# Optimization experiments

Hardware: AMD Instinct MI355X
Metric: run time of the kernel (lower is better)

The kernel has to match this reference:

```python
import jax, jax.numpy as jnp
import numpy as np

N_NODES = 50000
N_EDGES = 1600000
IN_FEATS = 128
HID = 128
HEADS = 4
F_HEAD = HID // HEADS  # 32
NEG_SLOPE = 0.2


def setup_inputs() -> dict:
    key = jax.random.key(0)
    ks = jax.random.split(key, 7)
    feat = jax.random.normal(ks[0], (N_NODES, IN_FEATS), dtype=jnp.float32)
    # Xavier-ish scaling for the shared fc weight
    W = jax.random.normal(ks[1], (IN_FEATS, HID), dtype=jnp.float32) * (1.0 / np.sqrt(IN_FEATS))
    attn_l = jax.random.normal(ks[2], (HEADS, F_HEAD), dtype=jnp.float32) * 0.1
    attn_r = jax.random.normal(ks[3], (HEADS, F_HEAD), dtype=jnp.float32) * 0.1
    bias = jnp.zeros((HID,), dtype=jnp.float32)
    src_idx = jax.random.randint(ks[4], (N_EDGES,), 0, N_NODES, dtype=jnp.int32)
    dst_idx = jax.random.randint(ks[5], (N_EDGES,), 0, N_NODES, dtype=jnp.int32)
    return {"feat": feat, "W": W, "attn_l": attn_l, "attn_r": attn_r,
            "bias": bias, "src_idx": src_idx, "dst_idx": dst_idx}


def reference(feat, W, attn_l, attn_r, bias, src_idx, dst_idx):
    N = feat.shape[0]
    # shared linear projection, split into heads: [N, H, F]
    ft = (feat @ W).reshape(N, HEADS, F_HEAD)
    # per-node attention logits: [N, H]
    el = jnp.einsum('nhf,hf->nh', ft, attn_l)
    er = jnp.einsum('nhf,hf->nh', ft, attn_r)
    # per-edge unnormalized score: [E, H]
    e = jax.nn.leaky_relu(el[src_idx] + er[dst_idx], negative_slope=NEG_SLOPE)
    # numerically stable edge softmax grouped by destination node
    m = jax.ops.segment_max(e, dst_idx, num_segments=N)          # [N, H]
    m = jnp.where(jnp.isfinite(m), m, 0.0)                       # guard empty dst
    a = jnp.exp(e - m[dst_idx])                                  # [E, H]
    s = jax.ops.segment_sum(a, dst_idx, num_segments=N)          # [N, H]
    alpha = a / jnp.where(s[dst_idx] > 0, s[dst_idx], 1.0)       # [E, H]
    # weighted scatter-sum aggregation: [N, H, F]
    msgs = ft[src_idx] * alpha[:, :, None]
    out = jax.ops.segment_sum(msgs, dst_idx, num_segments=N)
    out = out + bias.reshape(1, HEADS, F_HEAD)
    return out.reshape(N, HEADS * F_HEAD)  # flatten(1)
```

## Files before the change

### kernel.cpp

```cpp
#include <hip/hip_runtime.h>
#include <hip/hip_bf16.h>
#include <math.h>

#define NEG_SLOPE 0.2f
#define NBMAX 1024
#define CAP 4096
#define CH 8192

typedef __attribute__((ext_vector_type(8))) short short8;
typedef __attribute__((ext_vector_type(4))) float f32x4;
union BU { uint4 u; short8 s; };

__device__ __forceinline__ unsigned bf16rne(float f) {
    unsigned u = __float_as_uint(f);
    return (u + 0x7fffu + ((u >> 16) & 1u)) >> 16;
}
__device__ __forceinline__ short bf16s(float f) { return (short)bf16rne(f); }

__global__ __launch_bounds__(256) void k_wprep(
    const float* __restrict__ W, const float* __restrict__ attn_l,
    const float* __restrict__ attn_r, uint4* __restrict__ Wfrag,
    float4* __restrict__ WL, float4* __restrict__ WR,
    int* __restrict__ gcur, int NB) {
    int tid = blockIdx.x * 256 + threadIdx.x;
    if (tid < 2048) {
        int lane = tid & 63;
        int ki = (tid >> 6) & 3;
        int t = (tid >> 8) & 3;
        int cg = tid >> 10;
        int col = cg * 64 + t * 16 + (lane & 15);
        int kb = ki * 32 + (lane >> 4) * 8;
        unsigned d[4];
#pragma unroll
        for (int p = 0; p < 4; ++p) {
            unsigned lo = bf16rne(W[(kb + 2 * p) * 128 + col]);
            unsigned hi = bf16rne(W[(kb + 2 * p + 1) * 128 + col]);
            d[p] = lo | (hi << 16);
        }
        Wfrag[tid] = make_uint4(d[0], d[1], d[2], d[3]);
    } else if (tid < 2048 + 128) {
        int k = tid - 2048;
        const float* wr_ = W + k * 128;
        float l0 = 0, l1 = 0, l2 = 0, l3 = 0, r0 = 0, r1 = 0, r2 = 0, r3 = 0;
        for (int j = 0; j < 32; ++j) {
            l0 += wr_[j] * attn_l[j];
            l1 += wr_[32 + j] * attn_l[32 + j];
            l2 += wr_[64 + j] * attn_l[64 + j];
            l3 += wr_[96 + j] * attn_l[96 + j];
            r0 += wr_[j] * attn_r[j];
            r1 += wr_[32 + j] * attn_r[32 + j];
            r2 += wr_[64 + j] * attn_r[64 + j];
            r3 += wr_[96 + j] * attn_r[96 + j];
        }
        WL[k] = make_float4(l0, l1, l2, l3);
        WR[k] = make_float4(r0, r1, r2, r3);
    } else if (tid - 2176 < NB) {
        gcur[tid - 2176] = 0;
    }
}

__global__ __launch_bounds__(256) void k_fc(
    const float* __restrict__ feat, const uint4* __restrict__ Wfrag,
    const f32x4* __restrict__ WL, const f32x4* __restrict__ WR,
    unsigned* __restrict__ ftbf, float* __restrict__ el, float* __restrict__ er,
    int N) {
    __shared__ f32x4 WLs[128], WRs[128];
    int tid = threadIdx.x;
    if (tid < 128) WLs[tid] = WL[tid];
    else WRs[tid - 128] = WR[tid - 128];
    __syncthreads();
    const int wave = tid >> 6, lane = tid & 63;
    const int rt = wave & 1, cg = wave >> 1;
    const int nbase = blockIdx.x * 32 + rt * 16;
    const int row = nbase + (lane & 15);
    const int rowc = min(row, N - 1);
    const int q = lane >> 4;

    BU b[4][4];
#pragma unroll
    for (int t = 0; t < 4; ++t)
#pragma unroll
        for (int ki = 0; ki < 4; ++ki)
            b[t][ki].u = Wfrag[cg * 1024 + t * 256 + ki * 64 + lane];

    f32x4 acc0 = {0, 0, 0, 0}, acc1 = {0, 0, 0, 0}, acc2 = {0, 0, 0, 0}, acc3 = {0, 0, 0, 0};
    f32x4 elacc = {0, 0, 0, 0}, eracc = {0, 0, 0, 0};
    const float* fr = feat + (size_t)rowc * 128;
#pragma unroll
    for (int ki = 0; ki < 4; ++ki) {
        float4 f0 = *(const float4*)(fr + ki * 32 + q * 8);
        float4 f1 = *(const float4*)(fr + ki * 32 + q * 8 + 4);
        short8 a;
        a[0] = bf16s(f0.x); a[1] = bf16s(f0.y); a[2] = bf16s(f0.z); a[3] = bf16s(f0.w);
        a[4] = bf16s(f1.x); a[5] = bf16s(f1.y); a[6] = bf16s(f1.z); a[7] = bf16s(f1.w);
        acc0 = __builtin_amdgcn_mfma_f32_16x16x32_bf16(a, b[0][ki].s, acc0, 0, 0, 0);
        acc1 = __builtin_amdgcn_mfma_f32_16x16x32_bf16(a, b[1][ki].s, acc1, 0, 0, 0);
        acc2 = __builtin_amdgcn_mfma_f32_16x16x32_bf16(a, b[2][ki].s, acc2, 0, 0, 0);
        acc3 = __builtin_amdgcn_mfma_f32_16x16x32_bf16(a, b[3][ki].s, acc3, 0, 0, 0);
        if (cg == 0) {
            int kb = ki * 32 + q * 8;
            elacc += f0.x * WLs[kb + 0]; eracc += f0.x * WRs[kb + 0];
            elacc += f0.y * WLs[kb + 1]; eracc += f0.y * WRs[kb + 1];
            elacc += f0.z * WLs[kb + 2]; eracc += f0.z * WRs[kb + 2];
            elacc += f0.w * WLs[kb + 3]; eracc += f0.w * WRs[kb + 3];
            elacc += f1.x * WLs[kb + 4]; eracc += f1.x * WRs[kb + 4];
            elacc += f1.y * WLs[kb + 5]; eracc += f1.y * WRs[kb + 5];
            elacc += f1.z * WLs[kb + 6]; eracc += f1.z * WRs[kb + 6];
            elacc += f1.w * WLs[kb + 7]; eracc += f1.w * WRs[kb + 7];
        }
    }
#pragma unroll
    for (int t = 0; t < 4; ++t) {
#pragma unroll
        for (int r = 0; r < 4; ++r) {
            float d = (t == 0) ? acc0[r] : (t == 1) ? acc1[r] : (t == 2) ? acc2[r] : acc3[r];
            unsigned m = bf16rne(d);
            unsigned nb = (unsigned)__shfl_xor((int)m, 1, 64);
            int node = nbase + q * 4 + r;
            if (!(lane & 1) && node < N)
                ftbf[(size_t)node * 64 + cg * 32 + t * 8 + ((lane & 15) >> 1)] = m | (nb << 16);
        }
    }
    if (cg == 0) {
#pragma unroll
        for (int c = 0; c < 4; ++c) {
            elacc[c] += __shfl_xor(elacc[c], 16, 64);
            eracc[c] += __shfl_xor(eracc[c], 16, 64);
            elacc[c] += __shfl_xor(elacc[c], 32, 64);
            eracc[c] += __shfl_xor(eracc[c], 32, 64);
        }
        if (lane < 16 && row < N) {
            *(float4*)(el + (size_t)row * 4) = make_float4(elacc[0], elacc[1], elacc[2], elacc[3]);
            *(float4*)(er + (size_t)row * 4) = make_float4(eracc[0], eracc[1], eracc[2], eracc[3]);
        }
    }
}

__global__ __launch_bounds__(1024) void k_scatter_b(
    const int* __restrict__ src, const int* __restrict__ dst,
    int* __restrict__ gcur, unsigned* __restrict__ B, int E, int NB) {
    __shared__ int h[NBMAX];
    __shared__ int lc[NBMAX];
    int tid = threadIdx.x;
    for (int t = tid; t < NB; t += 1024) h[t] = 0;
    __syncthreads();
    int beg = blockIdx.x * CH;
    int end = min(beg + CH, E);
    for (int i = beg + tid; i < end; i += 1024) atomicAdd(&h[dst[i] >> 6], 1);
    __syncthreads();
    for (int t = tid; t < NB; t += 1024)
        lc[t] = (h[t] > 0) ? atomicAdd(&gcur[t], h[t]) : 0;
    __syncthreads();
    for (int i = beg + tid; i < end; i += 1024) {
        int d = dst[i];
        int pos = atomicAdd(&lc[d >> 6], 1);
        if (pos < CAP)
            B[(size_t)(d >> 6) * CAP + pos] = ((unsigned)src[i] << 6) | (unsigned)(d & 63);
    }
}

__global__ __launch_bounds__(256) void k_sort(
    const unsigned* __restrict__ B, const int* __restrict__ gcur,
    int* __restrict__ srt, uint2* __restrict__ od, int N) {
    __shared__ int hist[64];
    __shared__ int cur[64];
    const int tid = threadIdx.x;
    const int b = blockIdx.x;
    const int m = min(gcur[b], CAP);
    const size_t base = (size_t)b * CAP;
    if (tid < 64) hist[tid] = 0;
    __syncthreads();
    for (int i = tid; i < m; i += 256) atomicAdd(&hist[B[base + i] & 63], 1);
    __syncthreads();
    int v0 = (tid < 64) ? hist[tid] : 0;
    for (int off = 1; off < 64; off <<= 1) {
        int t = (tid < 64 && tid >= off) ? hist[tid - off] : 0;
        __syncthreads();
        if (tid < 64) hist[tid] += t;
        __syncthreads();
    }
    if (tid < 64) {
        int ex = hist[tid] - v0;
        cur[tid] = ex;
        int node = (b << 6) + tid;
        if (node < N) od[node] = make_uint2((unsigned)(base + ex), (unsigned)v0);
    }
    __syncthreads();
    for (int i = tid; i < m; i += 256) {
        unsigned p = B[base + i];
        int pos = atomicAdd(&cur[p & 63], 1);
        srt[base + pos] = (int)(p >> 6);
    }
}

__global__ __launch_bounds__(256) void k_aggregate(
    const unsigned* __restrict__ ftbf, const float* __restrict__ el,
    const float* __restrict__ er, const int* __restrict__ srt,
    const uint2* __restrict__ od, const float* __restrict__ bias,
    float* __restrict__ out, int N) {
    __shared__ float als[4][64][4];
    __shared__ int snl[4][64];
    const int wave = threadIdx.x >> 6;
    const int lane = threadIdx.x & 63;
    const int l15 = lane & 15;
    const int hd = l15 >> 2;
    const int g = lane >> 4;
    int node = blockIdx.x * 4 + wave;
    if (node >= N) return;
    uint2 o = od[node];
    int beg = (int)o.x, cnt = (int)o.y;
    float4 erd = *(const float4*)(er + (size_t)node * 4);
    const uint4* ftv = (const uint4*)ftbf;

    float s0 = 0.f, s1 = 0.f, s2 = 0.f, s3 = 0.f;
    float ac0 = 0, ac1 = 0, ac2 = 0, ac3 = 0, ac4 = 0, ac5 = 0, ac6 = 0, ac7 = 0;
    for (int tile = 0; tile < cnt; tile += 64) {
        int tc = min(64, cnt - tile);
        float a0 = 0.f, a1 = 0.f, a2 = 0.f, a3 = 0.f;
        int sn = 0;
        if (lane < tc) {
            sn = srt[beg + tile + lane];
            float4 a = *(const float4*)(el + (size_t)sn * 4);
            float e0 = a.x + erd.x; e0 = fmaxf(e0, NEG_SLOPE * e0);
            float e1 = a.y + erd.y; e1 = fmaxf(e1, NEG_SLOPE * e1);
            float e2 = a.z + erd.z; e2 = fmaxf(e2, NEG_SLOPE * e2);
            float e3 = a.w + erd.w; e3 = fmaxf(e3, NEG_SLOPE * e3);
            a0 = __expf(e0); a1 = __expf(e1);
            a2 = __expf(e2); a3 = __expf(e3);
        }
        s0 += a0; s1 += a1; s2 += a2; s3 += a3;
        *(float4*)(&als[wave][lane][0]) = make_float4(a0, a1, a2, a3);
        snl[wave][lane] = sn;
#pragma unroll 2
        for (int jj0 = 0; jj0 < tc; jj0 += 4) {
            int jj = jj0 + g;
            int j2 = (jj < tc) ? jj : (tc - 1);
            float af = als[wave][j2][hd];
            if (jj >= tc) af = 0.f;
            int s = snl[wave][j2];
            uint4 u = ftv[((size_t)s << 4) + l15];
            ac0 = fmaf(__uint_as_float(u.x << 16), af, ac0);
            ac1 = fmaf(__uint_as_float(u.x & 0xffff0000u), af, ac1);
            ac2 = fmaf(__uint_as_float(u.y << 16), af, ac2);
            ac3 = fmaf(__uint_as_float(u.y & 0xffff0000u), af, ac3);
            ac4 = fmaf(__uint_as_float(u.z << 16), af, ac4);
            ac5 = fmaf(__uint_as_float(u.z & 0xffff0000u), af, ac5);
            ac6 = fmaf(__uint_as_float(u.w << 16), af, ac6);
            ac7 = fmaf(__uint_as_float(u.w & 0xffff0000u), af, ac7);
        }
    }
#pragma unroll
    for (int off = 16; off <= 32; off <<= 1) {
        ac0 += __shfl_xor(ac0, off, 64);
        ac1 += __shfl_xor(ac1, off, 64);
        ac2 += __shfl_xor(ac2, off, 64);
        ac3 += __shfl_xor(ac3, off, 64);
        ac4 += __shfl_xor(ac4, off, 64);
        ac5 += __shfl_xor(ac5, off, 64);
        ac6 += __shfl_xor(ac6, off, 64);
        ac7 += __shfl_xor(ac7, off, 64);
    }
#pragma unroll
    for (int off = 32; off >= 1; off >>= 1) {
        s0 += __shfl_xor(s0, off, 64);
        s1 += __shfl_xor(s1, off, 64);
        s2 += __shfl_xor(s2, off, 64);
        s3 += __shfl_xor(s3, off, 64);
    }
    float ssel = (hd == 0) ? s0 : (hd == 1) ? s1 : (hd == 2) ? s2 : s3;
    float inv = ssel > 0.f ? 1.f / ssel : 0.f;
    if (lane < 16) {
        int c0 = lane * 8;
        float4 b0 = *(const float4*)(bias + c0);
        float4 b1 = *(const float4*)(bias + c0 + 4);
        float4 o0, o1;
        o0.x = ac0 * inv + b0.x; o0.y = ac1 * inv + b0.y;
        o0.z = ac2 * inv + b0.z; o0.w = ac3 * inv + b0.w;
        o1.x = ac4 * inv + b1.x; o1.y = ac5 * inv + b1.y;
        o1.z = ac6 * inv + b1.z; o1.w = ac7 * inv + b1.w;
        *(float4*)(out + (size_t)node * 128 + c0) = o0;
        *(float4*)(out + (size_t)node * 128 + c0 + 4) = o1;
    }
}

extern "C" void kernel_launch(void* const* d_in, const int* in_sizes, int n_in,
                              void* d_out, int out_size, void* d_ws, size_t ws_size,
                              hipStream_t stream) {
    const float* feat = (const float*)d_in[0];
    const float* W = (const float*)d_in[1];
    const float* attn_l = (const float*)d_in[2];
    const float* attn_r = (const float*)d_in[3];
    const float* bias = (const float*)d_in[4];
    const int* src = (const int*)d_in[5];
    const int* dst = (const int*)d_in[6];
    const int N = in_sizes[0] / 128;
    const int E = in_sizes[5];
    const int NB = (N + 63) >> 6;
    float* out = (float*)d_out;

    char* p = (char*)d_ws;
    unsigned int* ftbf = (unsigned int*)p;  p += (size_t)N * 64 * 4;
    unsigned* B = (unsigned*)p;             p += (size_t)NB * CAP * 4;
    int* srt = (int*)p;                     p += (size_t)NB * CAP * 4;
    float* el = (float*)p;                  p += (size_t)N * 4 * 4;
    float* er = (float*)p;                  p += (size_t)N * 4 * 4;
    uint2* od = (uint2*)p;                  p += (size_t)N * 8;
    int* gcur = (int*)p;                    p += ((size_t)NB * 4 + 15) & ~15ull;
    uint4* Wfrag = (uint4*)p;               p += 2048 * 16;
    float4* WL = (float4*)p;                p += 128 * 16;
    float4* WR = (float4*)p;                p += 128 * 16;

    int eblocks = (E + CH - 1) / CH;
    k_wprep<<<12, 256, 0, stream>>>(W, attn_l, attn_r, Wfrag, WL, WR, gcur, NB);
    k_fc<<<(N + 31) / 32, 256, 0, stream>>>(feat, Wfrag, (const f32x4*)WL,
                                            (const f32x4*)WR, ftbf, el, er, N);
    k_scatter_b<<<eblocks, 1024, 0, stream>>>(src, dst, gcur, B, E, NB);
    k_sort<<<NB, 256, 0, stream>>>(B, gcur, srt, od, N);
    k_aggregate<<<(N + 3) / 4, 256, 0, stream>>>(ftbf, el, er, srt, od, bias, out, N);
}
```

Measured before the change: 112.1 us.

## Prefetch gathered features in aggregate, cache dst in LDS, widen sort blocks

The aggregation loop is restructured to process eight edges per iteration with a software-prefetched double register buffer of gathered bf16 feature rows, using packed two-wide float FMAs and an occupancy hint of 8 blocks. The scatter kernel caches destination indices in shared memory so the second pass does not reload them from global memory. The sort kernel now runs with 512 threads per block. The intent is to hide gather latency and cut redundant loads, at the cost of more registers and 32KB of extra LDS in scatter.

```diff
diff --git a/kernel.cpp b/kernel.cpp
--- a/kernel.cpp
+++ b/kernel.cpp
@@ -9,6 +9,7 @@
 
 typedef __attribute__((ext_vector_type(8))) short short8;
 typedef __attribute__((ext_vector_type(4))) float f32x4;
+typedef __attribute__((ext_vector_type(2))) float f32x2;
 union BU { uint4 u; short8 s; };
 
 __device__ __forceinline__ unsigned bf16rne(float f) {
@@ -141,25 +142,30 @@
     int* __restrict__ gcur, unsigned* __restrict__ B, int E, int NB) {
     __shared__ int h[NBMAX];
     __shared__ int lc[NBMAX];
+    __shared__ int dl[CH];
     int tid = threadIdx.x;
     for (int t = tid; t < NB; t += 1024) h[t] = 0;
     __syncthreads();
     int beg = blockIdx.x * CH;
     int end = min(beg + CH, E);
-    for (int i = beg + tid; i < end; i += 1024) atomicAdd(&h[dst[i] >> 6], 1);
+    for (int i = beg + tid; i < end; i += 1024) {
+        int d = dst[i];
+        dl[i - beg] = d;
+        atomicAdd(&h[d >> 6], 1);
+    }
     __syncthreads();
     for (int t = tid; t < NB; t += 1024)
         lc[t] = (h[t] > 0) ? atomicAdd(&gcur[t], h[t]) : 0;
     __syncthreads();
     for (int i = beg + tid; i < end; i += 1024) {
-        int d = dst[i];
+        int d = dl[i - beg];
         int pos = atomicAdd(&lc[d >> 6], 1);
         if (pos < CAP)
             B[(size_t)(d >> 6) * CAP + pos] = ((unsigned)src[i] << 6) | (unsigned)(d & 63);
     }
 }
 
-__global__ __launch_bounds__(256) void k_sort(
+__global__ __launch_bounds__(512) void k_sort(
     const unsigned* __restrict__ B, const int* __restrict__ gcur,
     int* __restrict__ srt, uint2* __restrict__ od, int N) {
     __shared__ int hist[64];
@@ -170,7 +176,7 @@
     const size_t base = (size_t)b * CAP;
     if (tid < 64) hist[tid] = 0;
     __syncthreads();
-    for (int i = tid; i < m; i += 256) atomicAdd(&hist[B[base + i] & 63], 1);
+    for (int i = tid; i < m; i += 512) atomicAdd(&hist[B[base + i] & 63], 1);
     __syncthreads();
     int v0 = (tid < 64) ? hist[tid] : 0;
     for (int off = 1; off < 64; off <<= 1) {
@@ -186,14 +192,14 @@
         if (node < N) od[node] = make_uint2((unsigned)(base + ex), (unsigned)v0);
     }
     __syncthreads();
-    for (int i = tid; i < m; i += 256) {
+    for (int i = tid; i < m; i += 512) {
         unsigned p = B[base + i];
         int pos = atomicAdd(&cur[p & 63], 1);
         srt[base + pos] = (int)(p >> 6);
     }
 }
 
-__global__ __launch_bounds__(256) void k_aggregate(
+__global__ __launch_bounds__(256, 8) void k_aggregate(
     const unsigned* __restrict__ ftbf, const float* __restrict__ el,
     const float* __restrict__ er, const int* __restrict__ srt,
     const uint2* __restrict__ od, const float* __restrict__ bias,
@@ -213,9 +219,10 @@
     const uint4* ftv = (const uint4*)ftbf;
 
     float s0 = 0.f, s1 = 0.f, s2 = 0.f, s3 = 0.f;
-    float ac0 = 0, ac1 = 0, ac2 = 0, ac3 = 0, ac4 = 0, ac5 = 0, ac6 = 0, ac7 = 0;
+    f32x2 p0 = {0, 0}, p1 = {0, 0}, p2 = {0, 0}, p3 = {0, 0};
     for (int tile = 0; tile < cnt; tile += 64) {
         int tc = min(64, cnt - tile);
+        int tcm1 = tc - 1;
         float a0 = 0.f, a1 = 0.f, a2 = 0.f, a3 = 0.f;
         int sn = 0;
         if (lane < tc) {
@@ -231,34 +238,44 @@
         s0 += a0; s1 += a1; s2 += a2; s3 += a3;
         *(float4*)(&als[wave][lane][0]) = make_float4(a0, a1, a2, a3);
         snl[wave][lane] = sn;
-#pragma unroll 2
-        for (int jj0 = 0; jj0 < tc; jj0 += 4) {
-            int jj = jj0 + g;
-            int j2 = (jj < tc) ? jj : (tc - 1);
-            float af = als[wave][j2][hd];
-            if (jj >= tc) af = 0.f;
-            int s = snl[wave][j2];
-            uint4 u = ftv[((size_t)s << 4) + l15];
-            ac0 = fmaf(__uint_as_float(u.x << 16), af, ac0);
-            ac1 = fmaf(__uint_as_float(u.x & 0xffff0000u), af, ac1);
-            ac2 = fmaf(__uint_as_float(u.y << 16), af, ac2);
-            ac3 = fmaf(__uint_as_float(u.y & 0xffff0000u), af, ac3);
-            ac4 = fmaf(__uint_as_float(u.z << 16), af, ac4);
-            ac5 = fmaf(__uint_as_float(u.z & 0xffff0000u), af, ac5);
-            ac6 = fmaf(__uint_as_float(u.w << 16), af, ac6);
-            ac7 = fmaf(__uint_as_float(u.w & 0xffff0000u), af, ac7);
+        int sA = snl[wave][min(g, tcm1)];
+        int sB = snl[wave][min(4 + g, tcm1)];
+        uint4 uA = ftv[((size_t)sA << 4) + l15];
+        uint4 uB = ftv[((size_t)sB << 4) + l15];
+        for (int jj0 = 0; jj0 < tc; jj0 += 8) {
+            float afA = (jj0 + g < tc) ? als[wave][jj0 + g][hd] : 0.f;
+            float afB = (jj0 + 4 + g < tc) ? als[wave][jj0 + 4 + g][hd] : 0.f;
+            uint4 vA = uA, vB = uB;
+            if (jj0 + 8 < tc) {
+                int s = snl[wave][min(jj0 + 8 + g, tcm1)];
+                uA = ftv[((size_t)s << 4) + l15];
+            }
+            if (jj0 + 12 < tc) {
+                int s = snl[wave][min(jj0 + 12 + g, tcm1)];
+                uB = ftv[((size_t)s << 4) + l15];
+            }
+            {
+                f32x2 af2 = {afA, afA};
+                p0 += (f32x2){__uint_as_float(vA.x << 16), __uint_as_float(vA.x & 0xffff0000u)} * af2;
+                p1 += (f32x2){__uint_as_float(vA.y << 16), __uint_as_float(vA.y & 0xffff0000u)} * af2;
+                p2 += (f32x2){__uint_as_float(vA.z << 16), __uint_as_float(vA.z & 0xffff0000u)} * af2;
+                p3 += (f32x2){__uint_as_float(vA.w << 16), __uint_as_float(vA.w & 0xffff0000u)} * af2;
+            }
+            {
+                f32x2 af2 = {afB, afB};
+                p0 += (f32x2){__uint_as_float(vB.x << 16), __uint_as_float(vB.x & 0xffff0000u)} * af2;
+                p1 += (f32x2){__uint_as_float(vB.y << 16), __uint_as_float(vB.y & 0xffff0000u)} * af2;
+                p2 += (f32x2){__uint_as_float(vB.z << 16), __uint_as_float(vB.z & 0xffff0000u)} * af2;
+                p3 += (f32x2){__uint_as_float(vB.w << 16), __uint_as_float(vB.w & 0xffff0000u)} * af2;
+            }
         }
     }
 #pragma unroll
     for (int off = 16; off <= 32; off <<= 1) {
-        ac0 += __shfl_xor(ac0, off, 64);
-        ac1 += __shfl_xor(ac1, off, 64);
-        ac2 += __shfl_xor(ac2, off, 64);
-        ac3 += __shfl_xor(ac3, off, 64);
-        ac4 += __shfl_xor(ac4, off, 64);
-        ac5 += __shfl_xor(ac5, off, 64);
-        ac6 += __shfl_xor(ac6, off, 64);
-        ac7 += __shfl_xor(ac7, off, 64);
+        p0.x += __shfl_xor(p0.x, off, 64); p0.y += __shfl_xor(p0.y, off, 64);
+        p1.x += __shfl_xor(p1.x, off, 64); p1.y += __shfl_xor(p1.y, off, 64);
+        p2.x += __shfl_xor(p2.x, off, 64); p2.y += __shfl_xor(p2.y, off, 64);
+        p3.x += __shfl_xor(p3.x, off, 64); p3.y += __shfl_xor(p3.y, off, 64);
     }
 #pragma unroll
     for (int off = 32; off >= 1; off >>= 1) {
@@ -274,10 +291,10 @@
         float4 b0 = *(const float4*)(bias + c0);
         float4 b1 = *(const float4*)(bias + c0 + 4);
         float4 o0, o1;
-        o0.x = ac0 * inv + b0.x; o0.y = ac1 * inv + b0.y;
-        o0.z = ac2 * inv + b0.z; o0.w = ac3 * inv + b0.w;
-        o1.x = ac4 * inv + b1.x; o1.y = ac5 * inv + b1.y;
-        o1.z = ac6 * inv + b1.z; o1.w = ac7 * inv + b1.w;
+        o0.x = p0.x * inv + b0.x; o0.y = p0.y * inv + b0.y;
+        o0.z = p1.x * inv + b0.z; o0.w = p1.y * inv + b0.w;
+        o1.x = p2.x * inv + b1.x; o1.y = p2.y * inv + b1.y;
+        o1.z = p3.x * inv + b1.z; o1.w = p3.y * inv + b1.w;
         *(float4*)(out + (size_t)node * 128 + c0) = o0;
         *(float4*)(out + (size_t)node * 128 + c0 + 4) = o1;
     }
@@ -315,6 +332,6 @@
     k_fc<<<(N + 31) / 32, 256, 0, stream>>>(feat, Wfrag, (const f32x4*)WL,
                                             (const f32x4*)WR, ftbf, el, er, N);
     k_scatter_b<<<eblocks, 1024, 0, stream>>>(src, dst, gcur, B, E, NB);
-    k_sort<<<NB, 256, 0, stream>>>(B, gcur, srt, od, N);
+    k_sort<<<NB, 512, 0, stream>>>(B, gcur, srt, od, N);
     k_aggregate<<<(N + 3) / 4, 256, 0, stream>>>(ftbf, el, er, srt, od, bias, out, N);
 }
```

Measured after the change: 111.3 us. About the same (-0.7%).
